# Kernel optimization log

Hardware: AMD Instinct MI355X
Metric: run time of the kernel (lower is better)

## Reference

```python
import jax, jax.numpy as jnp
import numpy as np


def setup_inputs() -> dict:
    key = jax.random.key(0)
    k1, k2 = jax.random.split(key)
    B, L, D = 8, 2048, 128
    x1 = jax.random.normal(k1, (B, L, D), dtype=jnp.float32)
    x2 = jax.random.normal(k2, (B, L, D), dtype=jnp.float32)
    return {"x1": x1, "x2": x2}


def reference(x1, x2):
    # attention[b, i, j] = <x1[b,i,:], x2[b,j,:]>   -> [B, L1, L2]
    attention = jnp.einsum("bid,bjd->bij", x1, x2)
    # softmax over axis=1 (rows / L1) and axis=2 (cols / L2)
    w_att_1 = jax.nn.softmax(attention, axis=1)              # [B, L1, L2]
    w_att_2 = jnp.swapaxes(jax.nn.softmax(attention, axis=2), 1, 2)  # [B, L2, L1]
    # Dot(axes=1): contract the sequence axis 1
    in1_aligned = jnp.einsum("bij,bid->bjd", w_att_1, x1)    # [B, L2, D]
    in2_aligned = jnp.einsum("bji,bjd->bid", w_att_2, x2)    # [B, L1, D]
    # submult(a, b) = concat([a - b, a * b]); combined = concat([a, b, a-b, a*b])
    q1_combined = jnp.concatenate(
        [x1, in2_aligned, x1 - in2_aligned, x1 * in2_aligned], axis=-1)  # [B, L1, 4D]
    q2_combined = jnp.concatenate(
        [x2, in1_aligned, x2 - in1_aligned, x2 * in1_aligned], axis=-1)  # [B, L2, 4D]
    return q1_combined, q2_combined
```

## Files before the change

### kernel.cpp

```cpp
#include <hip/hip_runtime.h>


typedef __bf16    bf16;
typedef _Float16  f16;
typedef __bf16    bf16x4 __attribute__((ext_vector_type(4)));
typedef _Float16  f16x4  __attribute__((ext_vector_type(4)));
typedef __bf16    bf16x8 __attribute__((ext_vector_type(8)));
typedef _Float16  f16x8  __attribute__((ext_vector_type(8)));
typedef float     floatx4 __attribute__((ext_vector_type(4)));
typedef unsigned int uintx4 __attribute__((ext_vector_type(4)));

#define NB 8
#define SL 2048
#define TI 32
#define NT 32

#define F16SZ (NB * SL * 128 * 2)

#define SKV_S  136
#define SVT_S  32

#define OFF_VT   8704
#define GSPAN    16896
#define OFF_L    33792
#define LDS_BYTES 33920

__global__ __launch_bounds__(256)
void prepass_cvt(const float* __restrict__ x1, const float* __restrict__ x2,
                 char* __restrict__ ws)
{
    __shared__ float tile[64 * 129];
    const int tid = threadIdx.x;
    const int j0  = blockIdx.x * 64;
    const int b   = blockIdx.y;
    const int z   = blockIdx.z;
    const float* src = z ? x2 : x1;
    f16*  oF = (f16*) (ws + (size_t)z * F16SZ);
    bf16* oT = (bf16*)(ws + 2 * (size_t)F16SZ + (size_t)z * F16SZ);

    #pragma unroll
    for (int n = 0; n < 8; ++n) {
        int ci = n * 256 + tid;
        int row = ci >> 5, c4 = ci & 31;
        const float4 v = *(const float4*)(src + ((size_t)b * SL + j0 + row) * 128 + c4 * 4);
        tile[row * 129 + c4 * 4 + 0] = v.x;
        tile[row * 129 + c4 * 4 + 1] = v.y;
        tile[row * 129 + c4 * 4 + 2] = v.z;
        tile[row * 129 + c4 * 4 + 3] = v.w;
        f16x4 h; h[0] = (f16)v.x; h[1] = (f16)v.y; h[2] = (f16)v.z; h[3] = (f16)v.w;
        *(f16x4*)(oF + ((size_t)b * SL + j0 + row) * 128 + c4 * 4) = h;
    }
    __syncthreads();
    #pragma unroll
    for (int n = 0; n < 8; ++n) {
        int fi = n * 256 + tid;
        int jg = fi & 15, d = fi >> 4;
        bf16x4 o;
        #pragma unroll
        for (int i = 0; i < 4; ++i) o[i] = (bf16)tile[(jg * 4 + i) * 129 + d];
        *(bf16x4*)(oT + ((size_t)b * 128 + d) * SL + j0 + jg * 4) = o;
    }
}

__global__ __launch_bounds__(256, 4)
void soft_attn_align_mfma(const float* __restrict__ x1,
                          const float* __restrict__ x2,
                          const char* __restrict__ ws,
                          float* __restrict__ out)
{
    __shared__ __align__(16) char lds_raw[LDS_BYTES];

    const int tid  = threadIdx.x;
    const int lane = tid & 63;
    const int wv   = tid >> 6;
    const int g    = wv >> 1;
    const int rowbase = (wv & 1) * 16;
    const int lr   = lane & 15;
    const int lq   = lane >> 4;
    const int t128 = tid & 127;

    char* gb  = lds_raw + g * GSPAN;
    f16*  sKV = (f16*) (gb);
    bf16* sVT = (bf16*)(gb + OFF_VT);
    float* aOut = (float*)(lds_raw);
    float* sL   = (float*)(lds_raw + OFF_L);

    const int i0  = blockIdx.x * TI;
    const int bi  = blockIdx.y;
    const int dir = blockIdx.z;

    const float* xq = dir ? x2 : x1;
    const f16*  x1f = (const f16*)(ws);
    const f16*  x2f = (const f16*)(ws + F16SZ);
    const bf16* x1T = (const bf16*)(ws + 2 * (size_t)F16SZ);
    const bf16* x2T = (const bf16*)(ws + 3 * (size_t)F16SZ);
    const f16*  xqf  = dir ? x2f : x1f;
    const f16*  xkvf = dir ? x1f : x2f;
    const bf16* xvT  = dir ? x1T : x2T;

    f16x8 aQ[4];
    {
        const f16* qrow = xqf + ((size_t)bi * SL + i0 + rowbase + lr) * 128;
        #pragma unroll
        for (int kk = 0; kk < 4; ++kk)
            aQ[kk] = *(const f16x8*)(qrow + kk * 32 + lq * 8);
    }

    float   l_acc = 0.0f;
    floatx4 Oacc[8];
    #pragma unroll
    for (int nd = 0; nd < 8; ++nd) Oacc[nd] = (floatx4){0.f, 0.f, 0.f, 0.f};

    const int rowK = t128 >> 4, colK = t128 & 15;
    const int dV0  = t128 >> 2, jcV  = t128 & 3;
    const f16*  kvf = xkvf + ((size_t)bi * SL + g * 1024 + rowK) * 128 + colK * 8;
    const bf16* vTf = xvT + ((size_t)bi * 128 + dV0) * SL + g * 1024 + jcV * 8;

    f16x8  kreg[4];
    bf16x8 vreg[4];
    {
        #pragma unroll
        for (int n = 0; n < 4; ++n) {
            kreg[n] = *(const f16x8*)(kvf + (size_t)n * 8 * 128);
            vreg[n] = *(const bf16x8*)(vTf + (size_t)n * 32 * SL);
        }
    }

    for (int t = 0; t < NT; ++t) {
        __syncthreads();

        #pragma unroll
        for (int n = 0; n < 4; ++n) {
            *(f16x8*) (sKV + (rowK + n * 8) * SKV_S + colK * 8) = kreg[n];
            *(bf16x8*)(sVT + (dV0 + n * 32) * SVT_S + jcV * 8)  = vreg[n];
        }
        __syncthreads();

        if (t < NT - 1) {
            const f16*  kb = kvf + (size_t)(t + 1) * 32 * 128;
            const bf16* vb = vTf + (size_t)(t + 1) * 32;
            #pragma unroll
            for (int n = 0; n < 4; ++n) {
                kreg[n] = *(const f16x8*)(kb + (size_t)n * 8 * 128);
                vreg[n] = *(const bf16x8*)(vb + (size_t)n * 32 * SL);
            }
        }

        floatx4 Sf0 = (floatx4){0.f, 0.f, 0.f, 0.f};
        floatx4 Sf1 = (floatx4){0.f, 0.f, 0.f, 0.f};
        __builtin_amdgcn_s_setprio(1);
        #pragma unroll
        for (int kk = 0; kk < 4; ++kk) {
            f16x8 aK0 = *(const f16x8*)(sKV + (lr)      * SKV_S + kk * 32 + lq * 8);
            f16x8 aK1 = *(const f16x8*)(sKV + (16 + lr) * SKV_S + kk * 32 + lq * 8);
            Sf0 = __builtin_amdgcn_mfma_f32_16x16x32_f16(aK0, aQ[kk], Sf0, 0, 0, 0);
            Sf1 = __builtin_amdgcn_mfma_f32_16x16x32_f16(aK1, aQ[kk], Sf1, 0, 0, 0);
        }
        __builtin_amdgcn_s_setprio(0);

        float p00 = __expf(Sf0[0]), p01 = __expf(Sf0[1]);
        float p02 = __expf(Sf0[2]), p03 = __expf(Sf0[3]);
        float p10 = __expf(Sf1[0]), p11 = __expf(Sf1[1]);
        float p12 = __expf(Sf1[2]), p13 = __expf(Sf1[3]);
        l_acc += ((p00 + p01) + (p02 + p03)) + ((p10 + p11) + (p12 + p13));

        unsigned int A0, B0, A1, B1;
        asm("v_cvt_pk_bf16_f32 %0, %1, %2" : "=v"(A0) : "v"(p00), "v"(p01));
        asm("v_cvt_pk_bf16_f32 %0, %1, %2" : "=v"(B0) : "v"(p02), "v"(p03));
        asm("v_cvt_pk_bf16_f32 %0, %1, %2" : "=v"(A1) : "v"(p10), "v"(p11));
        asm("v_cvt_pk_bf16_f32 %0, %1, %2" : "=v"(B1) : "v"(p12), "v"(p13));
        asm("v_permlane32_swap_b32 %0, %1" : "+v"(A0), "+v"(A1));
        asm("v_permlane16_swap_b32 %0, %1" : "+v"(A0), "+v"(A1));
        asm("v_permlane32_swap_b32 %0, %1" : "+v"(B0), "+v"(B1));
        asm("v_permlane16_swap_b32 %0, %1" : "+v"(B0), "+v"(B1));
        uintx4 fr; fr.x = A0; fr.y = B0; fr.z = A1; fr.w = B1;
        bf16x8 aP = __builtin_bit_cast(bf16x8, fr);

        __builtin_amdgcn_s_setprio(1);
        #pragma unroll
        for (int nd = 0; nd < 8; ++nd) {
            bf16x8 bV = *(const bf16x8*)(sVT + (nd * 16 + lr) * SVT_S + lq * 8);
            Oacc[nd] = __builtin_amdgcn_mfma_f32_16x16x32_bf16(aP, bV, Oacc[nd], 0, 0, 0);
        }
        __builtin_amdgcn_s_setprio(0);
    }

    l_acc += __shfl_xor(l_acc, 16, 64);
    l_acc += __shfl_xor(l_acc, 32, 64);
    float l_row[4];
    #pragma unroll
    for (int r = 0; r < 4; ++r)
        l_row[r] = __shfl(l_acc, lq * 4 + r, 64);

    __syncthreads();

    if (g == 1) {
        #pragma unroll
        for (int r = 0; r < 4; ++r) {
            int row = rowbase + lq * 4 + r;
            #pragma unroll
            for (int nd = 0; nd < 8; ++nd)
                aOut[row * 132 + nd * 16 + lr] = Oacc[nd][r];
            if (lr == 0) sL[row] = l_row[r];
        }
    }
    __syncthreads();
    if (g == 0) {
        #pragma unroll
        for (int r = 0; r < 4; ++r) {
            int row = rowbase + lq * 4 + r;
            float inv = 1.0f / (l_row[r] + sL[row]);
            #pragma unroll
            for (int nd = 0; nd < 8; ++nd) {
                int idx = row * 132 + nd * 16 + lr;
                aOut[idx] = (Oacc[nd][r] + aOut[idx]) * inv;
            }
        }
    }
    __syncthreads();

    float* outb = out + ((size_t)dir * NB * SL + (size_t)bi * SL + i0) * 512;
    #pragma unroll
    for (int k = 0; k < 4; ++k) {
        int s = tid + 256 * k;
        int r = s >> 5, c4 = s & 31;
        float4 a = *(const float4*)(aOut + r * 132 + c4 * 4);
        float4 q = *(const float4*)(xq + ((size_t)bi * SL + i0 + r) * 128 + c4 * 4);
        float4 d, m;
        d.x = q.x - a.x; d.y = q.y - a.y; d.z = q.z - a.z; d.w = q.w - a.w;
        m.x = q.x * a.x; m.y = q.y * a.y; m.z = q.z * a.z; m.w = q.w * a.w;
        float4* orow = (float4*)(outb + (size_t)r * 512);
        orow[c4]      = q;
        orow[32 + c4] = a;
        orow[64 + c4] = d;
        orow[96 + c4] = m;
    }
}

extern "C" void kernel_launch(void* const* d_in, const int* in_sizes, int n_in,
                              void* d_out, int out_size, void* d_ws, size_t ws_size,
                              hipStream_t stream) {
    const float* x1 = (const float*)d_in[0];
    const float* x2 = (const float*)d_in[1];
    float* out = (float*)d_out;
    (void)in_sizes; (void)n_in; (void)out_size; (void)ws_size;

    dim3 pgrid(SL / 64, NB, 2);
    prepass_cvt<<<pgrid, dim3(256), 0, stream>>>(x1, x2, (char*)d_ws);

    dim3 grid(SL / TI, NB, 2);
    soft_attn_align_mfma<<<grid, dim3(256), 0, stream>>>(x1, x2, (const char*)d_ws, out);
}
```

Measured before the change: 148.5 us.

## Double query rows per wave, feed K from registers, swizzle block order

Each wave now handles 32 query rows instead of 16, so each K and V fragment serves two MFMA row tiles. K fragments are loaded straight from global memory into double-buffered registers (aKA/aKB), which removes the K staging in LDS and one set of LDS reads. Block indices are remapped with a swizzle to group blocks sharing a batch for better L2 locality. In exchange, register pressure roughly doubles, launch bounds drop to 2 blocks per CU, and K loads are no longer coalesced through LDS.

```diff
diff --git a/kernel.cpp b/kernel.cpp
--- a/kernel.cpp
+++ b/kernel.cpp
@@ -12,18 +12,16 @@
 
 #define NB 8
 #define SL 2048
-#define TI 32
+#define TI 64
 #define NT 32
 
 #define F16SZ (NB * SL * 128 * 2)
 
-#define SKV_S  136
 #define SVT_S  32
 
-#define OFF_VT   8704
-#define GSPAN    16896
+#define GSPAN    8192
 #define OFF_L    33792
-#define LDS_BYTES 33920
+#define LDS_BYTES 34048
 
 __global__ __launch_bounds__(256)
 void prepass_cvt(const float* __restrict__ x1, const float* __restrict__ x2,
@@ -62,7 +60,85 @@
     }
 }
 
-__global__ __launch_bounds__(256, 4)
+#define TILE_BODY(T, AKC, AKN)                                                     \
+    {                                                                              \
+        __syncthreads();          \
+        _Pragma("unroll")                                                          \
+        for (int n = 0; n < 4; ++n)                                                \
+            *(bf16x8*)(sVT + (dV0 + n * 32) * SVT_S + jcV * 8) = vreg[n];          \
+        __syncthreads();                                    \
+        if ((T) < NT - 1) {                                                        \
+            const f16*  kb = kfp + (size_t)((T) + 1) * 32 * 128;                   \
+            const bf16* vb = vTf + (size_t)((T) + 1) * 32;                         \
+            _Pragma("unroll")                                                      \
+            for (int h = 0; h < 2; ++h)                                            \
+                _Pragma("unroll")                                                  \
+                for (int kk = 0; kk < 4; ++kk)                                     \
+                    AKN[h * 4 + kk] = *(const f16x8*)(kb + h * 2048 + kk * 32);    \
+            _Pragma("unroll")                                                      \
+            for (int n = 0; n < 4; ++n)                                            \
+                vreg[n] = *(const bf16x8*)(vb + (size_t)n * 32 * SL);              \
+        }                                                                          \
+        floatx4 Sf[2][2];                                                          \
+        Sf[0][0] = (floatx4){0.f,0.f,0.f,0.f}; Sf[0][1] = (floatx4){0.f,0.f,0.f,0.f}; \
+        Sf[1][0] = (floatx4){0.f,0.f,0.f,0.f}; Sf[1][1] = (floatx4){0.f,0.f,0.f,0.f}; \
+        __builtin_amdgcn_s_setprio(1);                                             \
+        _Pragma("unroll")                                                          \
+        for (int kk = 0; kk < 4; ++kk) {                                           \
+            Sf[0][0] = __builtin_amdgcn_mfma_f32_16x16x32_f16(AKC[kk],     aQ[kk],  Sf[0][0], 0, 0, 0); \
+            Sf[0][1] = __builtin_amdgcn_mfma_f32_16x16x32_f16(AKC[4 + kk], aQ[kk],  Sf[0][1], 0, 0, 0); \
+            Sf[1][0] = __builtin_amdgcn_mfma_f32_16x16x32_f16(AKC[kk],     aQ2[kk], Sf[1][0], 0, 0, 0); \
+            Sf[1][1] = __builtin_amdgcn_mfma_f32_16x16x32_f16(AKC[4 + kk], aQ2[kk], Sf[1][1], 0, 0, 0); \
+        }                                                                          \
+        __builtin_amdgcn_s_setprio(0);                                             \
+        bf16x8 aP0, aP1;                                                           \
+        {                                                                          \
+            float p00 = __expf(Sf[0][0][0]), p01 = __expf(Sf[0][0][1]);            \
+            float p02 = __expf(Sf[0][0][2]), p03 = __expf(Sf[0][0][3]);            \
+            float p10 = __expf(Sf[0][1][0]), p11 = __expf(Sf[0][1][1]);            \
+            float p12 = __expf(Sf[0][1][2]), p13 = __expf(Sf[0][1][3]);            \
+            l_acc += ((p00 + p01) + (p02 + p03)) + ((p10 + p11) + (p12 + p13));    \
+            unsigned int A0, B0, A1, B1;                                           \
+            asm("v_cvt_pk_bf16_f32 %0, %1, %2" : "=v"(A0) : "v"(p00), "v"(p01));   \
+            asm("v_cvt_pk_bf16_f32 %0, %1, %2" : "=v"(B0) : "v"(p02), "v"(p03));   \
+            asm("v_cvt_pk_bf16_f32 %0, %1, %2" : "=v"(A1) : "v"(p10), "v"(p11));   \
+            asm("v_cvt_pk_bf16_f32 %0, %1, %2" : "=v"(B1) : "v"(p12), "v"(p13));   \
+            asm("v_permlane32_swap_b32 %0, %1" : "+v"(A0), "+v"(A1));              \
+            asm("v_permlane16_swap_b32 %0, %1" : "+v"(A0), "+v"(A1));              \
+            asm("v_permlane32_swap_b32 %0, %1" : "+v"(B0), "+v"(B1));              \
+            asm("v_permlane16_swap_b32 %0, %1" : "+v"(B0), "+v"(B1));              \
+            uintx4 fr; fr.x = A0; fr.y = B0; fr.z = A1; fr.w = B1;                 \
+            aP0 = __builtin_bit_cast(bf16x8, fr);                                  \
+        }                                                                          \
+        {                                                                          \
+            float p00 = __expf(Sf[1][0][0]), p01 = __expf(Sf[1][0][1]);            \
+            float p02 = __expf(Sf[1][0][2]), p03 = __expf(Sf[1][0][3]);            \
+            float p10 = __expf(Sf[1][1][0]), p11 = __expf(Sf[1][1][1]);            \
+            float p12 = __expf(Sf[1][1][2]), p13 = __expf(Sf[1][1][3]);            \
+            l_acc2 += ((p00 + p01) + (p02 + p03)) + ((p10 + p11) + (p12 + p13));   \
+            unsigned int A0, B0, A1, B1;                                           \
+            asm("v_cvt_pk_bf16_f32 %0, %1, %2" : "=v"(A0) : "v"(p00), "v"(p01));   \
+            asm("v_cvt_pk_bf16_f32 %0, %1, %2" : "=v"(B0) : "v"(p02), "v"(p03));   \
+            asm("v_cvt_pk_bf16_f32 %0, %1, %2" : "=v"(A1) : "v"(p10), "v"(p11));   \
+            asm("v_cvt_pk_bf16_f32 %0, %1, %2" : "=v"(B1) : "v"(p12), "v"(p13));   \
+            asm("v_permlane32_swap_b32 %0, %1" : "+v"(A0), "+v"(A1));              \
+            asm("v_permlane16_swap_b32 %0, %1" : "+v"(A0), "+v"(A1));              \
+            asm("v_permlane32_swap_b32 %0, %1" : "+v"(B0), "+v"(B1));              \
+            asm("v_permlane16_swap_b32 %0, %1" : "+v"(B0), "+v"(B1));              \
+            uintx4 fr; fr.x = A0; fr.y = B0; fr.z = A1; fr.w = B1;                 \
+            aP1 = __builtin_bit_cast(bf16x8, fr);                                  \
+        }                                                                          \
+        __builtin_amdgcn_s_setprio(1);                                             \
+        _Pragma("unroll")                                                          \
+        for (int nd = 0; nd < 8; ++nd) {                                           \
+            bf16x8 bV = *(const bf16x8*)(sVT + (nd * 16 + lr) * SVT_S + lq * 8);   \
+            Oacc[nd]  = __builtin_amdgcn_mfma_f32_16x16x32_bf16(aP0, bV, Oacc[nd],  0, 0, 0); \
+            Oacc2[nd] = __builtin_amdgcn_mfma_f32_16x16x32_bf16(aP1, bV, Oacc2[nd], 0, 0, 0); \
+        }                                                                          \
+        __builtin_amdgcn_s_setprio(0);                                             \
+    }
+
+__global__ __launch_bounds__(256, 2)
 void soft_attn_align_mfma(const float* __restrict__ x1,
                           const float* __restrict__ x2,
                           const char* __restrict__ ws,
@@ -74,20 +150,21 @@
     const int lane = tid & 63;
     const int wv   = tid >> 6;
     const int g    = wv >> 1;
-    const int rowbase = (wv & 1) * 16;
+    const int rowbase = (wv & 1) * 32;
     const int lr   = lane & 15;
     const int lq   = lane >> 4;
     const int t128 = tid & 127;
 
-    char* gb  = lds_raw + g * GSPAN;
-    f16*  sKV = (f16*) (gb);
-    bf16* sVT = (bf16*)(gb + OFF_VT);
+    bf16* sVT  = (bf16*)(lds_raw + g * GSPAN);
     float* aOut = (float*)(lds_raw);
     float* sL   = (float*)(lds_raw + OFF_L);
 
-    const int i0  = blockIdx.x * TI;
-    const int bi  = blockIdx.y;
-    const int dir = blockIdx.z;
+    const int lid = blockIdx.x + 32 * (blockIdx.y + 8 * blockIdx.z);
+    const int swz = (lid & 7) * 64 + (lid >> 3);
+    const int ix  = swz & 31;
+    const int bi  = (swz >> 5) & 7;
+    const int dir = swz >> 8;
+    const int i0  = ix * TI;
 
     const float* xq = dir ? x2 : x1;
     const f16*  x1f = (const f16*)(ws);
@@ -98,130 +175,95 @@
     const f16*  xkvf = dir ? x1f : x2f;
     const bf16* xvT  = dir ? x1T : x2T;
 
-    f16x8 aQ[4];
+    f16x8 aQ[4], aQ2[4];
     {
-        const f16* qrow = xqf + ((size_t)bi * SL + i0 + rowbase + lr) * 128;
+        const f16* qrow0 = xqf + ((size_t)bi * SL + i0 + rowbase + 0  + lr) * 128;
+        const f16* qrow1 = xqf + ((size_t)bi * SL + i0 + rowbase + 16 + lr) * 128;
+        #pragma unroll
+        for (int kk = 0; kk < 4; ++kk) {
+            aQ[kk]  = *(const f16x8*)(qrow0 + kk * 32 + lq * 8);
+            aQ2[kk] = *(const f16x8*)(qrow1 + kk * 32 + lq * 8);
+        }
+    }
+    float l_acc = 0.0f, l_acc2 = 0.0f;
+    floatx4 Oacc[8], Oacc2[8];
+    #pragma unroll
+    for (int nd = 0; nd < 8; ++nd) {
+        Oacc[nd]  = (floatx4){0.f, 0.f, 0.f, 0.f};
+        Oacc2[nd] = (floatx4){0.f, 0.f, 0.f, 0.f};
+    }
+
+    const int dV0 = t128 >> 2, jcV = t128 & 3;
+    const bf16* vTf = xvT + ((size_t)bi * 128 + dV0) * SL + g * 1024 + jcV * 8;
+    const f16* kfp = xkvf + ((size_t)bi * SL + g * 1024 + lr) * 128 + lq * 8;
+
+    f16x8  aKA[8], aKB[8];
+    bf16x8 vreg[4];
+    #pragma unroll
+    for (int h = 0; h < 2; ++h)
         #pragma unroll
         for (int kk = 0; kk < 4; ++kk)
-            aQ[kk] = *(const f16x8*)(qrow + kk * 32 + lq * 8);
-    }
-
-    float   l_acc = 0.0f;
-    floatx4 Oacc[8];
-    #pragma unroll
-    for (int nd = 0; nd < 8; ++nd) Oacc[nd] = (floatx4){0.f, 0.f, 0.f, 0.f};
-
-    const int rowK = t128 >> 4, colK = t128 & 15;
-    const int dV0  = t128 >> 2, jcV  = t128 & 3;
-    const f16*  kvf = xkvf + ((size_t)bi * SL + g * 1024 + rowK) * 128 + colK * 8;
-    const bf16* vTf = xvT + ((size_t)bi * 128 + dV0) * SL + g * 1024 + jcV * 8;
-
-    f16x8  kreg[4];
-    bf16x8 vreg[4];
+            aKA[h * 4 + kk] = *(const f16x8*)(kfp + h * 2048 + kk * 32);
+    #pragma unroll
+    for (int n = 0; n < 4; ++n)
+        vreg[n] = *(const bf16x8*)(vTf + (size_t)n * 32 * SL);
+
+    for (int t = 0; t < NT; t += 2) {
+        TILE_BODY(t,     aKA, aKB)
+        TILE_BODY(t + 1, aKB, aKA)
+    }
+
+    float l_row[2][4];
     {
-        #pragma unroll
-        for (int n = 0; n < 4; ++n) {
-            kreg[n] = *(const f16x8*)(kvf + (size_t)n * 8 * 128);
-            vreg[n] = *(const bf16x8*)(vTf + (size_t)n * 32 * SL);
+        float lv = l_acc;
+        lv += __shfl_xor(lv, 16, 64);
+        lv += __shfl_xor(lv, 32, 64);
+        #pragma unroll
+        for (int r = 0; r < 4; ++r) l_row[0][r] = __shfl(lv, lq * 4 + r, 64);
+        lv = l_acc2;
+        lv += __shfl_xor(lv, 16, 64);
+        lv += __shfl_xor(lv, 32, 64);
+        #pragma unroll
+        for (int r = 0; r < 4; ++r) l_row[1][r] = __shfl(lv, lq * 4 + r, 64);
+    }
+
+    __syncthreads();
+
+    if (g == 1) {
+        #pragma unroll
+        for (int r = 0; r < 4; ++r) {
+            int row0 = rowbase + lq * 4 + r;
+            int row1 = rowbase + 16 + lq * 4 + r;
+            #pragma unroll
+            for (int nd = 0; nd < 8; ++nd) {
+                aOut[row0 * 132 + nd * 16 + lr] = Oacc[nd][r];
+                aOut[row1 * 132 + nd * 16 + lr] = Oacc2[nd][r];
+            }
+            if (lr == 0) { sL[row0] = l_row[0][r]; sL[row1] = l_row[1][r]; }
         }
     }
-
-    for (int t = 0; t < NT; ++t) {
-        __syncthreads();
-
-        #pragma unroll
-        for (int n = 0; n < 4; ++n) {
-            *(f16x8*) (sKV + (rowK + n * 8) * SKV_S + colK * 8) = kreg[n];
-            *(bf16x8*)(sVT + (dV0 + n * 32) * SVT_S + jcV * 8)  = vreg[n];
-        }
-        __syncthreads();
-
-        if (t < NT - 1) {
-            const f16*  kb = kvf + (size_t)(t + 1) * 32 * 128;
-            const bf16* vb = vTf + (size_t)(t + 1) * 32;
+    __syncthreads();
+    if (g == 0) {
+        #pragma unroll
+        for (int r = 0; r < 4; ++r) {
+            int row0 = rowbase + lq * 4 + r;
+            int row1 = rowbase + 16 + lq * 4 + r;
+            float inv0 = 1.0f / (l_row[0][r] + sL[row0]);
+            float inv1 = 1.0f / (l_row[1][r] + sL[row1]);
             #pragma unroll
-            for (int n = 0; n < 4; ++n) {
-                kreg[n] = *(const f16x8*)(kb + (size_t)n * 8 * 128);
-                vreg[n] = *(const bf16x8*)(vb + (size_t)n * 32 * SL);
+            for (int nd = 0; nd < 8; ++nd) {
+                int idx0 = row0 * 132 + nd * 16 + lr;
+                int idx1 = row1 * 132 + nd * 16 + lr;
+                aOut[idx0] = (Oacc[nd][r]  + aOut[idx0]) * inv0;
+                aOut[idx1] = (Oacc2[nd][r] + aOut[idx1]) * inv1;
             }
         }
-
-        floatx4 Sf0 = (floatx4){0.f, 0.f, 0.f, 0.f};
-        floatx4 Sf1 = (floatx4){0.f, 0.f, 0.f, 0.f};
-        __builtin_amdgcn_s_setprio(1);
-        #pragma unroll
-        for (int kk = 0; kk < 4; ++kk) {
-            f16x8 aK0 = *(const f16x8*)(sKV + (lr)      * SKV_S + kk * 32 + lq * 8);
-            f16x8 aK1 = *(const f16x8*)(sKV + (16 + lr) * SKV_S + kk * 32 + lq * 8);
-            Sf0 = __builtin_amdgcn_mfma_f32_16x16x32_f16(aK0, aQ[kk], Sf0, 0, 0, 0);
-            Sf1 = __builtin_amdgcn_mfma_f32_16x16x32_f16(aK1, aQ[kk], Sf1, 0, 0, 0);
-        }
-        __builtin_amdgcn_s_setprio(0);
-
-        float p00 = __expf(Sf0[0]), p01 = __expf(Sf0[1]);
-        float p02 = __expf(Sf0[2]), p03 = __expf(Sf0[3]);
-        float p10 = __expf(Sf1[0]), p11 = __expf(Sf1[1]);
-        float p12 = __expf(Sf1[2]), p13 = __expf(Sf1[3]);
-        l_acc += ((p00 + p01) + (p02 + p03)) + ((p10 + p11) + (p12 + p13));
-
-        unsigned int A0, B0, A1, B1;
-        asm("v_cvt_pk_bf16_f32 %0, %1, %2" : "=v"(A0) : "v"(p00), "v"(p01));
-        asm("v_cvt_pk_bf16_f32 %0, %1, %2" : "=v"(B0) : "v"(p02), "v"(p03));
-        asm("v_cvt_pk_bf16_f32 %0, %1, %2" : "=v"(A1) : "v"(p10), "v"(p11));
-        asm("v_cvt_pk_bf16_f32 %0, %1, %2" : "=v"(B1) : "v"(p12), "v"(p13));
-        asm("v_permlane32_swap_b32 %0, %1" : "+v"(A0), "+v"(A1));
-        asm("v_permlane16_swap_b32 %0, %1" : "+v"(A0), "+v"(A1));
-        asm("v_permlane32_swap_b32 %0, %1" : "+v"(B0), "+v"(B1));
-        asm("v_permlane16_swap_b32 %0, %1" : "+v"(B0), "+v"(B1));
-        uintx4 fr; fr.x = A0; fr.y = B0; fr.z = A1; fr.w = B1;
-        bf16x8 aP = __builtin_bit_cast(bf16x8, fr);
-
-        __builtin_amdgcn_s_setprio(1);
-        #pragma unroll
-        for (int nd = 0; nd < 8; ++nd) {
-            bf16x8 bV = *(const bf16x8*)(sVT + (nd * 16 + lr) * SVT_S + lq * 8);
-            Oacc[nd] = __builtin_amdgcn_mfma_f32_16x16x32_bf16(aP, bV, Oacc[nd], 0, 0, 0);
-        }
-        __builtin_amdgcn_s_setprio(0);
-    }
-
-    l_acc += __shfl_xor(l_acc, 16, 64);
-    l_acc += __shfl_xor(l_acc, 32, 64);
-    float l_row[4];
-    #pragma unroll
-    for (int r = 0; r < 4; ++r)
-        l_row[r] = __shfl(l_acc, lq * 4 + r, 64);
-
-    __syncthreads();
-
-    if (g == 1) {
-        #pragma unroll
-        for (int r = 0; r < 4; ++r) {
-            int row = rowbase + lq * 4 + r;
-            #pragma unroll
-            for (int nd = 0; nd < 8; ++nd)
-                aOut[row * 132 + nd * 16 + lr] = Oacc[nd][r];
-            if (lr == 0) sL[row] = l_row[r];
-        }
-    }
-    __syncthreads();
-    if (g == 0) {
-        #pragma unroll
-        for (int r = 0; r < 4; ++r) {
-            int row = rowbase + lq * 4 + r;
-            float inv = 1.0f / (l_row[r] + sL[row]);
-            #pragma unroll
-            for (int nd = 0; nd < 8; ++nd) {
-                int idx = row * 132 + nd * 16 + lr;
-                aOut[idx] = (Oacc[nd][r] + aOut[idx]) * inv;
-            }
-        }
     }
     __syncthreads();
 
     float* outb = out + ((size_t)dir * NB * SL + (size_t)bi * SL + i0) * 512;
     #pragma unroll
-    for (int k = 0; k < 4; ++k) {
+    for (int k = 0; k < 8; ++k) {
         int s = tid + 256 * k;
         int r = s >> 5, c4 = s & 31;
         float4 a = *(const float4*)(aOut + r * 132 + c4 * 4);
```

Result: slower. 164.0 us (+10.5%).
